# Optimization experiments

Hardware: AMD Instinct MI355X
Metric: run time of the kernel (lower is better)

The kernel has to match this reference:

```python
import jax, jax.numpy as jnp
import numpy as np

BS, T, ND, DS, IN, H = 512, 100, 10, 6, 256, 256
SA = IN * ND + H  # 2816, attention MLP width


def setup_inputs() -> dict:
    key = jax.random.key(0)
    ks = jax.random.split(key, 8)
    def lin(k, out_d, in_d):
        return jax.random.normal(k, (out_d, in_d), jnp.float32) * (1.0 / np.sqrt(in_d)).astype(np.float32)
    return {
        "descriptors": jax.random.normal(ks[0], (BS, T, ND, DS), jnp.float32),
        "Wd": lin(ks[1], IN, DS), "bd": jnp.zeros((IN,), jnp.float32),
        "W1": lin(ks[2], SA, SA), "b1": jnp.zeros((SA,), jnp.float32),
        "W2": lin(ks[3], IN, SA), "b2": jnp.zeros((IN,), jnp.float32),
        "Wv": lin(ks[4], ND, SA), "bv": jnp.zeros((ND,), jnp.float32),
        "W_ih": lin(ks[5], 4 * H, IN), "W_hh": lin(ks[6], 4 * H, H),
        "b_ih": jnp.zeros((4 * H,), jnp.float32), "b_hh": jnp.zeros((4 * H,), jnp.float32),
    }


def reference(descriptors, Wd, bd, W1, b1, W2, b2, Wv, bv, W_ih, W_hh, b_ih, b_hh):
    bs = descriptors.shape[0]
    dt = descriptors.dtype
    desc_tm = jnp.swapaxes(descriptors, 0, 1)  # [T, bs, ND, DS] time-major for scan
    h0 = jnp.zeros((bs, H), dt)
    c0 = jnp.zeros((bs, H), dt)
    inp0 = jnp.zeros((bs, IN), dt)

    def step(carry, d):
        h, c, inp = carry
        # torch.nn.LSTMCell: gate order i, f, g, o
        gates = inp @ W_ih.T + b_ih + h @ W_hh.T + b_hh  # [bs, 4H]
        i, f, g, o = jnp.split(gates, 4, axis=-1)
        c = jax.nn.sigmoid(f) * c + jax.nn.sigmoid(i) * jnp.tanh(g)
        h = jax.nn.sigmoid(o) * jnp.tanh(c)
        # FrameAttention
        emb = d @ Wd.T + bd                               # [bs, ND, IN]
        x = jnp.concatenate([emb.reshape(bs, ND * IN), h], axis=-1)  # [bs, SA]
        x = jax.nn.relu(x @ W1.T + b1)
        nxt = jax.nn.relu(x @ W2.T + b2)
        a = x @ Wv.T + bv  # training mode: no sigmoid
        return (h, c, nxt), a

    _, att = jax.lax.scan(step, (h0, c0, inp0), desc_tm)  # att: [T, bs, ND]
    return jnp.swapaxes(att, 0, 1)  # [bs, T, ND]
```

## Files before the change

kernel.cpp:

```cpp
#include <hip/hip_runtime.h>
#include <hip/hip_bf16.h>
#include <math.h>

#define TT 100
#define ND 10
#define DS 6
#define SAW 2816

typedef _Float16 half8 __attribute__((ext_vector_type(8)));
typedef float floatx4 __attribute__((ext_vector_type(4)));

template<int EPI>
__global__ __launch_bounds__(256) void gemm_s16(
    const _Float16* __restrict__ Ah, const _Float16* __restrict__ Al, int lda,
    const _Float16* __restrict__ Bh, const _Float16* __restrict__ Bl, int ldb,
    const float* __restrict__ bias,
    float* __restrict__ Cf, _Float16* __restrict__ Chi, _Float16* __restrict__ Clo,
    int ldc, int Kloc)
{
    __shared__ alignas(16) _Float16 sAh[64 * 32];
    __shared__ alignas(16) _Float16 sAl[64 * 32];
    __shared__ alignas(16) _Float16 sBh[64 * 32];
    __shared__ alignas(16) _Float16 sBl[64 * 32];

    const int tid = threadIdx.x;
    const int w = tid >> 6, l = tid & 63;
    const int m0 = blockIdx.x * 64, n0 = blockIdx.y * 64;
    const int koff = (EPI == 2) ? blockIdx.z * Kloc : 0;

    const int sr = 16 * w + (l >> 2);
    const int sc = (l & 3) * 8;
    const int sidx = sr * 32 + sc;
    const _Float16* gAh = Ah + (size_t)(m0 + sr) * lda + koff + sc;
    const _Float16* gAl = Al + (size_t)(m0 + sr) * lda + koff + sc;
    const _Float16* gBh = Bh + (size_t)(n0 + sr) * ldb + koff + sc;
    const _Float16* gBl = Bl + (size_t)(n0 + sr) * ldb + koff + sc;

    const int mw = (w >> 1) * 32, nw = (w & 1) * 32;
    const int fr = l & 15, fk = (l >> 4) * 8;

    floatx4 acc[2][2];
    const floatx4 z = {0.f, 0.f, 0.f, 0.f};
#pragma unroll
    for (int i = 0; i < 2; ++i)
#pragma unroll
        for (int j = 0; j < 2; ++j) acc[i][j] = z;

    half8 rAh = *(const half8*)gAh;
    half8 rAl = *(const half8*)gAl;
    half8 rBh = *(const half8*)gBh;
    half8 rBl = *(const half8*)gBl;

    for (int kt = 0; kt < Kloc; kt += 32) {
        *(half8*)&sAh[sidx] = rAh;
        *(half8*)&sAl[sidx] = rAl;
        *(half8*)&sBh[sidx] = rBh;
        *(half8*)&sBl[sidx] = rBl;
        __syncthreads();
        if (kt + 32 < Kloc) {
            rAh = *(const half8*)(gAh + kt + 32);
            rAl = *(const half8*)(gAl + kt + 32);
            rBh = *(const half8*)(gBh + kt + 32);
            rBl = *(const half8*)(gBl + kt + 32);
        }
        half8 aH[2], aL[2], bH[2], bL[2];
#pragma unroll
        for (int mf = 0; mf < 2; ++mf) {
            const int ro = (mw + mf * 16 + fr) * 32 + fk;
            aH[mf] = *(const half8*)&sAh[ro];
            aL[mf] = *(const half8*)&sAl[ro];
        }
#pragma unroll
        for (int nf = 0; nf < 2; ++nf) {
            const int ro = (nw + nf * 16 + fr) * 32 + fk;
            bH[nf] = *(const half8*)&sBh[ro];
            bL[nf] = *(const half8*)&sBl[ro];
        }
#pragma unroll
        for (int mf = 0; mf < 2; ++mf)
#pragma unroll
            for (int nf = 0; nf < 2; ++nf)
                acc[mf][nf] = __builtin_amdgcn_mfma_f32_16x16x32_f16(aH[mf], bH[nf], acc[mf][nf], 0, 0, 0);
#pragma unroll
        for (int mf = 0; mf < 2; ++mf)
#pragma unroll
            for (int nf = 0; nf < 2; ++nf)
                acc[mf][nf] = __builtin_amdgcn_mfma_f32_16x16x32_f16(aH[mf], bL[nf], acc[mf][nf], 0, 0, 0);
#pragma unroll
        for (int mf = 0; mf < 2; ++mf)
#pragma unroll
            for (int nf = 0; nf < 2; ++nf)
                acc[mf][nf] = __builtin_amdgcn_mfma_f32_16x16x32_f16(aL[mf], bH[nf], acc[mf][nf], 0, 0, 0);
        __syncthreads();
    }

    const int cr = (l >> 4) * 4, cc = l & 15;
#pragma unroll
    for (int nf = 0; nf < 2; ++nf) {
        const int col = n0 + nw + nf * 16 + cc;
        float bv = 0.f;
        if constexpr (EPI != 2) bv = bias[col];
#pragma unroll
        for (int mf = 0; mf < 2; ++mf) {
            const int row = m0 + mw + mf * 16 + cr;
#pragma unroll
            for (int r = 0; r < 4; ++r) {
                float v = acc[mf][nf][r] + bv;
                if constexpr (EPI == 0) {
                    Cf[(size_t)(row + r) * ldc + col] = v;
                } else if constexpr (EPI == 1) {
                    v = v > 0.f ? v : 0.f;
                    const _Float16 h = (_Float16)v;
                    Chi[(size_t)(row + r) * ldc + col] = h;
                    Clo[(size_t)(row + r) * ldc + col] = (_Float16)(v - (float)h);
                } else {
                    Cf[(size_t)blockIdx.z * (512 * 256) + (size_t)(row + r) * ldc + col] = v;
                }
            }
        }
    }
}

__global__ __launch_bounds__(256) void lstm_emb(
    const float* __restrict__ gates, float* __restrict__ cbuf,
    _Float16* __restrict__ zhi, _Float16* __restrict__ zlo,
    _Float16* __restrict__ xhi, _Float16* __restrict__ xlo,
    const float* __restrict__ desc, const float* __restrict__ Wd,
    const float* __restrict__ bd, int t)
{
    __shared__ float sd[60];
    __shared__ float swd[1536];
    const int b = blockIdx.x, k = threadIdx.x;
    if (k < 60) sd[k] = desc[(size_t)b * (TT * ND * DS) + t * (ND * DS) + k];
    for (int i = k; i < 1536; i += 256) swd[i] = Wd[i];

    const float gi = gates[b * 1024 + k];
    const float gf = gates[b * 1024 + 256 + k];
    const float gg = gates[b * 1024 + 512 + k];
    const float go = gates[b * 1024 + 768 + k];
    const float si = 1.f / (1.f + expf(-gi));
    const float sf = 1.f / (1.f + expf(-gf));
    const float so = 1.f / (1.f + expf(-go));
    float cv = cbuf[b * 256 + k];
    cv = sf * cv + si * tanhf(gg);
    const float hv = so * tanhf(cv);
    cbuf[b * 256 + k] = cv;
    {
        const _Float16 h = (_Float16)hv;
        const _Float16 lo = (_Float16)(hv - (float)h);
        zhi[b * 512 + 256 + k] = h;   zlo[b * 512 + 256 + k] = lo;
        xhi[(size_t)b * SAW + 2560 + k] = h;
        xlo[(size_t)b * SAW + 2560 + k] = lo;
    }
    __syncthreads();

    const float bdv = bd[k];
#pragma unroll
    for (int n = 0; n < ND; ++n) {
        float a = bdv;
#pragma unroll
        for (int d = 0; d < DS; ++d) a += sd[n * DS + d] * swd[k * DS + d];
        const _Float16 h = (_Float16)a;
        xhi[(size_t)b * SAW + n * 256 + k] = h;
        xlo[(size_t)b * SAW + n * 256 + k] = (_Float16)(a - (float)h);
    }
}

__global__ __launch_bounds__(256) void av_w2fin(
    const _Float16* __restrict__ yhi, const _Float16* __restrict__ ylo,
    const float* __restrict__ Wv, const float* __restrict__ bv,
    const float* __restrict__ pbuf, const float* __restrict__ b2,
    _Float16* __restrict__ zhi, _Float16* __restrict__ zlo,
    float* __restrict__ out, int t)
{
    __shared__ float ys[SAW];
    __shared__ float red[ND][4];
    const int b = blockIdx.x, tid = threadIdx.x;
    for (int i = tid; i < SAW; i += 256)
        ys[i] = (float)yhi[(size_t)b * SAW + i] + (float)ylo[(size_t)b * SAW + i];
    __syncthreads();

    float pacc[ND];
#pragma unroll
    for (int n = 0; n < ND; ++n) pacc[n] = 0.f;
    for (int kk = tid; kk < SAW; kk += 256) {
        const float yv = ys[kk];
#pragma unroll
        for (int n = 0; n < ND; ++n) pacc[n] += yv * Wv[n * SAW + kk];
    }
    const int lane = tid & 63, wid = tid >> 6;
#pragma unroll
    for (int n = 0; n < ND; ++n) {
        float v = pacc[n];
        for (int off = 32; off > 0; off >>= 1) v += __shfl_down(v, off, 64);
        if (lane == 0) red[n][wid] = v;
    }
    {
        const int j = tid;
        float s = b2[j];
#pragma unroll
        for (int kc = 0; kc < 4; ++kc) s += pbuf[kc * 131072 + b * 256 + j];
        s = s > 0.f ? s : 0.f;
        const _Float16 h = (_Float16)s;
        zhi[b * 512 + j] = h;
        zlo[b * 512 + j] = (_Float16)(s - (float)h);
    }
    __syncthreads();
    if (tid < ND) {
        const float s = red[tid][0] + red[tid][1] + red[tid][2] + red[tid][3] + bv[tid];
        out[(size_t)b * (TT * ND) + t * ND + tid] = s;
    }
}

__global__ void build_wcat_split(const float* __restrict__ W_ih, const float* __restrict__ W_hh,
                                 const float* __restrict__ b_ih, const float* __restrict__ b_hh,
                                 _Float16* __restrict__ wchi, _Float16* __restrict__ wclo,
                                 float* __restrict__ bcat)
{
    const int j = blockIdx.x, k = threadIdx.x;
    const float v1 = W_ih[j * 256 + k];
    const _Float16 h1 = (_Float16)v1;
    wchi[j * 512 + k] = h1;
    wclo[j * 512 + k] = (_Float16)(v1 - (float)h1);
    const float v2 = W_hh[j * 256 + k];
    const _Float16 h2 = (_Float16)v2;
    wchi[j * 512 + 256 + k] = h2;
    wclo[j * 512 + 256 + k] = (_Float16)(v2 - (float)h2);
    if (k == 0) bcat[j] = b_ih[j] + b_hh[j];
}

__global__ __launch_bounds__(256) void cvt_hilo(const float* __restrict__ src,
                                                _Float16* __restrict__ hi,
                                                _Float16* __restrict__ lo, int n)
{
    int i = blockIdx.x * 256 + threadIdx.x;
    const int stride = gridDim.x * 256;
    for (; i < n; i += stride) {
        const float v = src[i];
        const _Float16 h = (_Float16)v;
        hi[i] = h;
        lo[i] = (_Float16)(v - (float)h);
    }
}

extern "C" void kernel_launch(void* const* d_in, const int* in_sizes, int n_in,
                              void* d_out, int out_size, void* d_ws, size_t ws_size,
                              hipStream_t stream)
{
    const float* desc = (const float*)d_in[0];
    const float* Wd   = (const float*)d_in[1];
    const float* bd   = (const float*)d_in[2];
    const float* W1   = (const float*)d_in[3];
    const float* b1   = (const float*)d_in[4];
    const float* W2   = (const float*)d_in[5];
    const float* b2   = (const float*)d_in[6];
    const float* Wv   = (const float*)d_in[7];
    const float* bv   = (const float*)d_in[8];
    const float* W_ih = (const float*)d_in[9];
    const float* W_hh = (const float*)d_in[10];
    const float* b_ih = (const float*)d_in[11];
    const float* b_hh = (const float*)d_in[12];
    float* out = (float*)d_out;

    char* ws = (char*)d_ws;
    _Float16* zhi  = (_Float16*)(ws);
    _Float16* zlo  = (_Float16*)(ws + 524288);
    float*    cbuf = (float*)(ws + 1048576);
    _Float16* xhi  = (_Float16*)(ws + 1572864);
    _Float16* xlo  = (_Float16*)(ws + 4456448);
    float*    pbuf = (float*)(ws + 1572864);
    _Float16* yhi  = (_Float16*)(ws + 7340032);
    _Float16* ylo  = (_Float16*)(ws + 10223616);
    float*    gates= (float*)(ws + 7340032);
    _Float16* wchi = (_Float16*)(ws + 13107200);
    _Float16* wclo = (_Float16*)(ws + 14155776);
    _Float16* w2hi = (_Float16*)(ws + 15204352);
    _Float16* w2lo = (_Float16*)(ws + 16646144);
    _Float16* w1hi = (_Float16*)(ws + 18087936);
    _Float16* w1lo = (_Float16*)(ws + 33947648);
    float*    bcat = (float*)(ws + 49807360);

    hipMemsetAsync(ws, 0, 1572864, stream);
    build_wcat_split<<<dim3(1024), dim3(256), 0, stream>>>(W_ih, W_hh, b_ih, b_hh,
                                                           wchi, wclo, bcat);
    cvt_hilo<<<dim3(4096), dim3(256), 0, stream>>>(W1, w1hi, w1lo, SAW * SAW);
    cvt_hilo<<<dim3(704), dim3(256), 0, stream>>>(W2, w2hi, w2lo, 256 * SAW);

    for (int t = 0; t < TT; ++t) {
        gemm_s16<0><<<dim3(8, 16), dim3(256), 0, stream>>>(
            zhi, zlo, 512, wchi, wclo, 512, bcat, gates, nullptr, nullptr, 1024, 512);
        lstm_emb<<<dim3(512), dim3(256), 0, stream>>>(gates, cbuf, zhi, zlo, xhi, xlo,
                                                      desc, Wd, bd, t);
        gemm_s16<1><<<dim3(8, 44), dim3(256), 0, stream>>>(
            xhi, xlo, SAW, w1hi, w1lo, SAW, b1, nullptr, yhi, ylo, SAW, SAW);
        gemm_s16<2><<<dim3(8, 4, 4), dim3(256), 0, stream>>>(
            yhi, ylo, SAW, w2hi, w2lo, SAW, nullptr, pbuf, nullptr, nullptr, 256, 704);
        av_w2fin<<<dim3(512), dim3(256), 0, stream>>>(yhi, ylo, Wv, bv, pbuf, b2,
                                                      zhi, zlo, out, t);
    }
}
```

Before: 10.06 ms.

## Use 128x128 split-K MFMA GEMM with direct global-to-LDS loads for LSTM and W1

Adds a new GEMM kernel with 128x128 tiles, 4x4 MFMA fragments per wave and global_load_lds direct copies, one wave per hi/lo plane. The LSTM gate GEMM and the large W1 GEMM now use split-K over 4 slices that write fp32 partials, summed in lstm_emb and in a new yred kernel that also applies bias, ReLU and the hi/lo split. The goal is more data reuse per tile while keeping enough blocks to fill the CUs. The cost is extra partial-buffer traffic, one more kernel launch per timestep, and y now aliasing the x buffers.

Measured after the change: 8.738 ms. -13.2%, faster.

```diff
diff --git a/kernel.cpp b/kernel.cpp
--- a/kernel.cpp
+++ b/kernel.cpp
@@ -10,13 +10,99 @@
 typedef _Float16 half8 __attribute__((ext_vector_type(8)));
 typedef float floatx4 __attribute__((ext_vector_type(4)));
 
-template<int EPI>
-__global__ __launch_bounds__(256) void gemm_s16(
+__device__ __forceinline__ void gload_lds16(const _Float16* g, _Float16* l) {
+    __builtin_amdgcn_global_load_lds((const __attribute__((address_space(1))) void*)g,
+                                     (__attribute__((address_space(3))) void*)l, 16, 0, 0);
+}
+
+__global__ __launch_bounds__(256) void gemm_big(
     const _Float16* __restrict__ Ah, const _Float16* __restrict__ Al, int lda,
     const _Float16* __restrict__ Bh, const _Float16* __restrict__ Bl, int ldb,
-    const float* __restrict__ bias,
-    float* __restrict__ Cf, _Float16* __restrict__ Chi, _Float16* __restrict__ Clo,
-    int ldc, int Kloc)
+    float* __restrict__ Cpart, size_t zstride, int ldc, int Kloc)
+{
+    __shared__ alignas(16) _Float16 lds[4 * 128 * 32];
+
+    const int tid = threadIdx.x;
+    const int w = tid >> 6, l = tid & 63;
+    const int m0 = blockIdx.x * 128, n0 = blockIdx.y * 128;
+    const int koff = blockIdx.z * Kloc;
+
+    const _Float16* plane_src;
+    int plane_ld;
+    if (w == 0)      { plane_src = Ah + (size_t)m0 * lda; plane_ld = lda; }
+    else if (w == 1) { plane_src = Al + (size_t)m0 * lda; plane_ld = lda; }
+    else if (w == 2) { plane_src = Bh + (size_t)n0 * ldb; plane_ld = ldb; }
+    else             { plane_src = Bl + (size_t)n0 * ldb; plane_ld = ldb; }
+    const int srow_in_chunk = l >> 2;
+    const int scol = (l & 3) * 8;
+    _Float16* const lds_plane = lds + w * 4096;
+
+    const int wr = (w >> 1) * 64, wc = (w & 1) * 64;
+    const int fr = l & 15, fk = (l >> 4) * 8;
+
+    floatx4 acc[4][4];
+    const floatx4 z4 = {0.f, 0.f, 0.f, 0.f};
+#pragma unroll
+    for (int i = 0; i < 4; ++i)
+#pragma unroll
+        for (int j = 0; j < 4; ++j) acc[i][j] = z4;
+
+    for (int kt = 0; kt < Kloc; kt += 32) {
+        __syncthreads();
+#pragma unroll
+        for (int i = 0; i < 8; ++i) {
+            const int row = i * 16 + srow_in_chunk;
+            gload_lds16(plane_src + (size_t)row * plane_ld + koff + kt + scol,
+                        lds_plane + i * 512);
+        }
+        __syncthreads();
+
+        half8 aH[4], aL[4], bH[4], bL[4];
+#pragma unroll
+        for (int f = 0; f < 4; ++f) {
+            const int ra = (wr + f * 16 + fr) * 32 + fk;
+            const int rb = (wc + f * 16 + fr) * 32 + fk;
+            aH[f] = *(const half8*)&lds[ra];
+            aL[f] = *(const half8*)&lds[4096 + ra];
+            bH[f] = *(const half8*)&lds[8192 + rb];
+            bL[f] = *(const half8*)&lds[12288 + rb];
+        }
+#pragma unroll
+        for (int mf = 0; mf < 4; ++mf)
+#pragma unroll
+            for (int nf = 0; nf < 4; ++nf)
+                acc[mf][nf] = __builtin_amdgcn_mfma_f32_16x16x32_f16(aH[mf], bH[nf], acc[mf][nf], 0, 0, 0);
+#pragma unroll
+        for (int mf = 0; mf < 4; ++mf)
+#pragma unroll
+            for (int nf = 0; nf < 4; ++nf)
+                acc[mf][nf] = __builtin_amdgcn_mfma_f32_16x16x32_f16(aH[mf], bL[nf], acc[mf][nf], 0, 0, 0);
+#pragma unroll
+        for (int mf = 0; mf < 4; ++mf)
+#pragma unroll
+            for (int nf = 0; nf < 4; ++nf)
+                acc[mf][nf] = __builtin_amdgcn_mfma_f32_16x16x32_f16(aL[mf], bH[nf], acc[mf][nf], 0, 0, 0);
+    }
+
+    float* const Cz = Cpart + (size_t)blockIdx.z * zstride;
+    const int cr = (l >> 4) * 4, cc = l & 15;
+#pragma unroll
+    for (int mf = 0; mf < 4; ++mf) {
+        const int row = m0 + wr + mf * 16 + cr;
+#pragma unroll
+        for (int nf = 0; nf < 4; ++nf) {
+            const int col = n0 + wc + nf * 16 + cc;
+#pragma unroll
+            for (int r = 0; r < 4; ++r)
+                Cz[(size_t)(row + r) * ldc + col] = acc[mf][nf][r];
+        }
+    }
+}
+
+__global__ __launch_bounds__(256) void gemm_s16_part(
+    const _Float16* __restrict__ Ah, const _Float16* __restrict__ Al, int lda,
+    const _Float16* __restrict__ Bh, const _Float16* __restrict__ Bl, int ldb,
+    float* __restrict__ Cf, int ldc, int Kloc)
 {
     __shared__ alignas(16) _Float16 sAh[64 * 32];
     __shared__ alignas(16) _Float16 sAl[64 * 32];
@@ -26,7 +112,7 @@
     const int tid = threadIdx.x;
     const int w = tid >> 6, l = tid & 63;
     const int m0 = blockIdx.x * 64, n0 = blockIdx.y * 64;
-    const int koff = (EPI == 2) ? blockIdx.z * Kloc : 0;
+    const int koff = blockIdx.z * Kloc;
 
     const int sr = 16 * w + (l >> 2);
     const int sc = (l & 3) * 8;
@@ -98,31 +184,37 @@
 #pragma unroll
     for (int nf = 0; nf < 2; ++nf) {
         const int col = n0 + nw + nf * 16 + cc;
-        float bv = 0.f;
-        if constexpr (EPI != 2) bv = bias[col];
 #pragma unroll
         for (int mf = 0; mf < 2; ++mf) {
             const int row = m0 + mw + mf * 16 + cr;
 #pragma unroll
-            for (int r = 0; r < 4; ++r) {
-                float v = acc[mf][nf][r] + bv;
-                if constexpr (EPI == 0) {
-                    Cf[(size_t)(row + r) * ldc + col] = v;
-                } else if constexpr (EPI == 1) {
-                    v = v > 0.f ? v : 0.f;
-                    const _Float16 h = (_Float16)v;
-                    Chi[(size_t)(row + r) * ldc + col] = h;
-                    Clo[(size_t)(row + r) * ldc + col] = (_Float16)(v - (float)h);
-                } else {
-                    Cf[(size_t)blockIdx.z * (512 * 256) + (size_t)(row + r) * ldc + col] = v;
-                }
-            }
-        }
+            for (int r = 0; r < 4; ++r)
+                Cf[(size_t)blockIdx.z * (512 * 256) + (size_t)(row + r) * ldc + col]
+                    = acc[mf][nf][r];
+        }
+    }
+}
+
+__global__ __launch_bounds__(256) void yred(const float* __restrict__ pbufY,
+                                            const float* __restrict__ b1,
+                                            _Float16* __restrict__ yhi,
+                                            _Float16* __restrict__ ylo)
+{
+    const int b = blockIdx.x, tid = threadIdx.x;
+    for (int i = tid; i < SAW; i += 256) {
+        float s = b1[i];
+#pragma unroll
+        for (int z = 0; z < 4; ++z) s += pbufY[(size_t)z * 1441792 + (size_t)b * SAW + i];
+        s = s > 0.f ? s : 0.f;
+        const _Float16 h = (_Float16)s;
+        yhi[(size_t)b * SAW + i] = h;
+        ylo[(size_t)b * SAW + i] = (_Float16)(s - (float)h);
     }
 }
 
 __global__ __launch_bounds__(256) void lstm_emb(
-    const float* __restrict__ gates, float* __restrict__ cbuf,
+    const float* __restrict__ gpart, const float* __restrict__ b_ih,
+    const float* __restrict__ b_hh, float* __restrict__ cbuf,
     _Float16* __restrict__ zhi, _Float16* __restrict__ zlo,
     _Float16* __restrict__ xhi, _Float16* __restrict__ xlo,
     const float* __restrict__ desc, const float* __restrict__ Wd,
@@ -134,15 +226,20 @@
     if (k < 60) sd[k] = desc[(size_t)b * (TT * ND * DS) + t * (ND * DS) + k];
     for (int i = k; i < 1536; i += 256) swd[i] = Wd[i];
 
-    const float gi = gates[b * 1024 + k];
-    const float gf = gates[b * 1024 + 256 + k];
-    const float gg = gates[b * 1024 + 512 + k];
-    const float go = gates[b * 1024 + 768 + k];
-    const float si = 1.f / (1.f + expf(-gi));
-    const float sf = 1.f / (1.f + expf(-gf));
-    const float so = 1.f / (1.f + expf(-go));
+    float gate[4];
+#pragma unroll
+    for (int g = 0; g < 4; ++g) {
+        const int idx = g * 256 + k;
+        float s = b_ih[idx] + b_hh[idx];
+#pragma unroll
+        for (int z = 0; z < 4; ++z) s += gpart[z * 524288 + b * 1024 + idx];
+        gate[g] = s;
+    }
+    const float si = 1.f / (1.f + expf(-gate[0]));
+    const float sf = 1.f / (1.f + expf(-gate[1]));
+    const float so = 1.f / (1.f + expf(-gate[3]));
     float cv = cbuf[b * 256 + k];
-    cv = sf * cv + si * tanhf(gg);
+    cv = sf * cv + si * tanhf(gate[2]);
     const float hv = so * tanhf(cv);
     cbuf[b * 256 + k] = cv;
     {
@@ -213,9 +310,7 @@
 }
 
 __global__ void build_wcat_split(const float* __restrict__ W_ih, const float* __restrict__ W_hh,
-                                 const float* __restrict__ b_ih, const float* __restrict__ b_hh,
-                                 _Float16* __restrict__ wchi, _Float16* __restrict__ wclo,
-                                 float* __restrict__ bcat)
+                                 _Float16* __restrict__ wchi, _Float16* __restrict__ wclo)
 {
     const int j = blockIdx.x, k = threadIdx.x;
     const float v1 = W_ih[j * 256 + k];
@@ -226,7 +321,6 @@
     const _Float16 h2 = (_Float16)v2;
     wchi[j * 512 + 256 + k] = h2;
     wclo[j * 512 + 256 + k] = (_Float16)(v2 - (float)h2);
-    if (k == 0) bcat[j] = b_ih[j] + b_hh[j];
 }
 
 __global__ __launch_bounds__(256) void cvt_hilo(const float* __restrict__ src,
@@ -268,34 +362,35 @@
     float*    cbuf = (float*)(ws + 1048576);
     _Float16* xhi  = (_Float16*)(ws + 1572864);
     _Float16* xlo  = (_Float16*)(ws + 4456448);
-    float*    pbuf = (float*)(ws + 1572864);
-    _Float16* yhi  = (_Float16*)(ws + 7340032);
-    _Float16* ylo  = (_Float16*)(ws + 10223616);
-    float*    gates= (float*)(ws + 7340032);
-    _Float16* wchi = (_Float16*)(ws + 13107200);
-    _Float16* wclo = (_Float16*)(ws + 14155776);
-    _Float16* w2hi = (_Float16*)(ws + 15204352);
-    _Float16* w2lo = (_Float16*)(ws + 16646144);
-    _Float16* w1hi = (_Float16*)(ws + 18087936);
-    _Float16* w1lo = (_Float16*)(ws + 33947648);
-    float*    bcat = (float*)(ws + 49807360);
+    _Float16* yhi  = xhi;
+    _Float16* ylo  = xlo;
+    float*    gpart = (float*)(ws + 7340032);
+    float*    pbufY = (float*)(ws + 7340032);
+    float*    pbufW2= (float*)(ws + 7340032);
+    _Float16* wchi = (_Float16*)(ws + 30408704);
+    _Float16* wclo = (_Float16*)(ws + 31457280);
+    _Float16* w2hi = (_Float16*)(ws + 32505856);
+    _Float16* w2lo = (_Float16*)(ws + 33947648);
+    _Float16* w1hi = (_Float16*)(ws + 35389440);
+    _Float16* w1lo = (_Float16*)(ws + 51249152);
 
     hipMemsetAsync(ws, 0, 1572864, stream);
-    build_wcat_split<<<dim3(1024), dim3(256), 0, stream>>>(W_ih, W_hh, b_ih, b_hh,
-                                                           wchi, wclo, bcat);
+    build_wcat_split<<<dim3(1024), dim3(256), 0, stream>>>(W_ih, W_hh, wchi, wclo);
     cvt_hilo<<<dim3(4096), dim3(256), 0, stream>>>(W1, w1hi, w1lo, SAW * SAW);
     cvt_hilo<<<dim3(704), dim3(256), 0, stream>>>(W2, w2hi, w2lo, 256 * SAW);
 
     for (int t = 0; t < TT; ++t) {
-        gemm_s16<0><<<dim3(8, 16), dim3(256), 0, stream>>>(
-            zhi, zlo, 512, wchi, wclo, 512, bcat, gates, nullptr, nullptr, 1024, 512);
-        lstm_emb<<<dim3(512), dim3(256), 0, stream>>>(gates, cbuf, zhi, zlo, xhi, xlo,
+        gemm_big<<<dim3(4, 8, 4), dim3(256), 0, stream>>>(
+            zhi, zlo, 512, wchi, wclo, 512, gpart, 524288, 1024, 128);
+        lstm_emb<<<dim3(512), dim3(256), 0, stream>>>(gpart, b_ih, b_hh, cbuf,
+                                                      zhi, zlo, xhi, xlo,
                                                       desc, Wd, bd, t);
-        gemm_s16<1><<<dim3(8, 44), dim3(256), 0, stream>>>(
-            xhi, xlo, SAW, w1hi, w1lo, SAW, b1, nullptr, yhi, ylo, SAW, SAW);
-        gemm_s16<2><<<dim3(8, 4, 4), dim3(256), 0, stream>>>(
-            yhi, ylo, SAW, w2hi, w2lo, SAW, nullptr, pbuf, nullptr, nullptr, 256, 704);
-        av_w2fin<<<dim3(512), dim3(256), 0, stream>>>(yhi, ylo, Wv, bv, pbuf, b2,
+        gemm_big<<<dim3(4, 22, 4), dim3(256), 0, stream>>>(
+            xhi, xlo, SAW, w1hi, w1lo, SAW, pbufY, 1441792, SAW, 704);
+        yred<<<dim3(512), dim3(256), 0, stream>>>(pbufY, b1, yhi, ylo);
+        gemm_s16_part<<<dim3(8, 4, 4), dim3(256), 0, stream>>>(
+            yhi, ylo, SAW, w2hi, w2lo, SAW, pbufW2, 256, 704);
+        av_w2fin<<<dim3(512), dim3(256), 0, stream>>>(yhi, ylo, Wv, bv, pbufW2, b2,
                                                       zhi, zlo, out, t);
     }
 }
```
